# Kernel optimization log

Hardware: AMD Instinct MI355X
Metric: run time of the kernel (lower is better)

The kernel has to match this reference:

```python
import jax, jax.numpy as jnp
import numpy as np

N_NODES = 100000
N_EDGES = 1600000
N_FEAT = 128
HIDDEN = 128
N_CLASSES = 40


def gcn_conv(x, W, b, src, dst, norm, n):
    # PyG GCNConv: linear (no bias) -> gather src -> scale by sym norm -> scatter-add to dst -> + bias
    h = x @ W                      # [N, out]
    m = h[src] * norm[:, None]     # [E+N, out] gathered, normalized messages
    out = jax.ops.segment_sum(m, dst, num_segments=n)
    return out + b


def setup_inputs() -> dict:
    key = jax.random.key(0)
    ks = jax.random.split(key, 10)
    x = jax.random.normal(ks[0], (N_NODES, N_FEAT), dtype=jnp.float32)
    edge_index = jax.random.randint(ks[1], (2, N_EDGES), 0, N_NODES, dtype=jnp.int32)

    def lin(k, fan_in, fan_out):
        s = 1.0 / np.sqrt(fan_in)
        return (jax.random.uniform(k, (fan_in, fan_out), jnp.float32, -s, s))

    return {
        "x": x,
        "edge_index": edge_index,
        "W1": lin(ks[2], N_FEAT, HIDDEN), "b1": jnp.zeros((HIDDEN,), jnp.float32),
        "W2": lin(ks[3], HIDDEN, HIDDEN), "b2": jnp.zeros((HIDDEN,), jnp.float32),
        "W3": lin(ks[4], HIDDEN, HIDDEN), "b3": jnp.zeros((HIDDEN,), jnp.float32),
        "W4": lin(ks[5], HIDDEN, N_CLASSES), "b4": jnp.zeros((N_CLASSES,), jnp.float32),
    }


def reference(x, edge_index, W1, b1, W2, b2, W3, b3, W4, b4):
    n = x.shape[0]
    # add self-loops (PyG GCNConv default)
    loops = jnp.arange(n, dtype=edge_index.dtype)
    src = jnp.concatenate([edge_index[0], loops])
    dst = jnp.concatenate([edge_index[1], loops])
    # symmetric degree normalization: deg computed on destination index
    deg = jax.ops.segment_sum(jnp.ones_like(dst, x.dtype), dst, num_segments=n)
    dinv = jnp.where(deg > 0, jax.lax.rsqrt(deg), 0.0)
    norm = dinv[src] * dinv[dst]

    h = jax.nn.relu(gcn_conv(x, W1, b1, src, dst, norm, n))   # dropout = identity (eval)
    h = jax.nn.relu(gcn_conv(h, W2, b2, src, dst, norm, n))
    h = jax.nn.relu(gcn_conv(h, W3, b3, src, dst, norm, n))
    x_latent = h
    out = gcn_conv(h, W4, b4, src, dst, norm, n)
    return out, x_latent
```

## Files before the change

kernel.cpp:

```cpp
#include <hip/hip_runtime.h>
#include <hip/hip_bf16.h>
#include <hip/hip_fp16.h>


#define N_NODES 100000
#define N_EDGES 1600000

#define BSHIFT 7
#define BWIDTH 128
#define CELL_CAP 512
#define P1_EPT 16
#define P1_CHUNK 4096

typedef short s16x8 __attribute__((ext_vector_type(8)));
typedef _Float16 f16x8 __attribute__((ext_vector_type(8)));
typedef float f32x4 __attribute__((ext_vector_type(4)));
typedef float f32x2 __attribute__((ext_vector_type(2)));


__global__ __launch_bounds__(256) void pass1_bucket(const int* __restrict__ src,
                                                    const int* __restrict__ dst,
                                                    int* __restrict__ bcur2,
                                                    int2* __restrict__ cells,
                                                    int2* __restrict__ spill,
                                                    int* __restrict__ spillCnt,
                                                    int nb, int e) {
    __shared__ int hist[1024];
    __shared__ int base[1024];
    int t = threadIdx.x;
    int x = blockIdx.x & 7;
    int e0 = blockIdx.x * P1_CHUNK;

    for (int i = t; i < nb; i += 256) hist[i] = 0;
    __syncthreads();

    int ds[P1_EPT], ss[P1_EPT];
#pragma unroll
    for (int j = 0; j < P1_EPT; j++) {
        int i = e0 + j * 256 + t;
        if (i < e) {
            ds[j] = dst[i];
            ss[j] = src[i];
            atomicAdd(&hist[ds[j] >> BSHIFT], 1);
        } else {
            ds[j] = -1;
        }
    }
    __syncthreads();

    for (int i = t; i < nb; i += 256) {
        int h = hist[i];
        base[i] = (h > 0) ? atomicAdd(&bcur2[i * 8 + x], h) : 0;
        hist[i] = 0;
    }
    __syncthreads();

#pragma unroll
    for (int j = 0; j < P1_EPT; j++) {
        if (ds[j] >= 0) {
            int b = ds[j] >> BSHIFT;
            int r = atomicAdd(&hist[b], 1);
            int slot = base[b] + r;
            if (slot < CELL_CAP) {
                cells[(size_t)(b * 8 + x) * CELL_CAP + slot] = make_int2(ss[j], ds[j]);
            } else {
                int sp = atomicAdd(spillCnt, 1);
                spill[sp] = make_int2(ss[j], ds[j]);
            }
        }
    }
}

__global__ __launch_bounds__(256) void count_cells(const int* __restrict__ bcur2,
                                                   const int2* __restrict__ cells,
                                                   const int2* __restrict__ spill,
                                                   const int* __restrict__ spillCnt,
                                                   int* __restrict__ counts,
                                                   float* __restrict__ dinv,
                                                   int n) {
    __shared__ int cnt[BWIDTH];
    int b = blockIdx.x;
    int t = threadIdx.x;
    int nodeBase = b << BSHIFT;
    if (t < BWIDTH) cnt[t] = 0;
    __syncthreads();
    for (int x = 0; x < 8; x++) {
        int c = bcur2[b * 8 + x];
        if (c > CELL_CAP) c = CELL_CAP;
        const int2* cp = cells + (size_t)(b * 8 + x) * CELL_CAP;
        for (int s = t; s < c; s += 256) {
            atomicAdd(&cnt[cp[s].y - nodeBase], 1);
        }
    }
    int sc = *spillCnt;
    for (int s = t; s < sc; s += 256) {
        int d = spill[s].y;
        if ((d >> BSHIFT) == b) atomicAdd(&cnt[d - nodeBase], 1);
    }
    __syncthreads();
    if (t < BWIDTH) {
        int node = nodeBase + t;
        if (node < n) {
            int deg = cnt[t] + 1;
            counts[node] = deg;
            dinv[node] = 1.0f / sqrtf((float)deg);
        }
    }
}

__global__ __launch_bounds__(256) void scan_phase1(const int* __restrict__ counts,
                                                   int* __restrict__ blockSums, int n) {
    __shared__ int red[256];
    int t = threadIdx.x;
    int base = blockIdx.x * 1024 + t * 4;
    int s = 0;
    if (base + 3 < n) {
        int4 v = *(const int4*)(counts + base);
        s = ((v.x + 2) & ~3) + ((v.y + 2) & ~3) + ((v.z + 2) & ~3) + ((v.w + 2) & ~3);
    } else {
        for (int j = 0; j < 4; j++) if (base + j < n) s += (counts[base + j] + 2) & ~3;
    }
    red[t] = s;
    __syncthreads();
    for (int off = 128; off > 0; off >>= 1) {
        if (t < off) red[t] += red[t + off];
        __syncthreads();
    }
    if (t == 0) blockSums[blockIdx.x] = red[0];
}

__global__ __launch_bounds__(1024) void scan_phase2(int* __restrict__ blockSums, int nb) {
    __shared__ int sh[1024];
    int t = threadIdx.x;
    sh[t] = (t < nb) ? blockSums[t] : 0;
    __syncthreads();
    for (int off = 1; off < 1024; off <<= 1) {
        int v = (t >= off) ? sh[t - off] : 0;
        __syncthreads();
        sh[t] += v;
        __syncthreads();
    }
    if (t < nb) blockSums[t] = (t == 0) ? 0 : sh[t - 1];
}

__global__ __launch_bounds__(256) void scan_phase3(const int* __restrict__ counts,
                                                   const int* __restrict__ blockSums,
                                                   int* __restrict__ offsets, int n) {
    __shared__ int red[256];
    int t = threadIdx.x;
    int base = blockIdx.x * 1024 + t * 4;
    int c[4];
#pragma unroll
    for (int j = 0; j < 4; j++) c[j] = (base + j < n) ? ((counts[base + j] + 2) & ~3) : 0;
    int s = c[0] + c[1] + c[2] + c[3];
    red[t] = s;
    __syncthreads();
    for (int off = 1; off < 256; off <<= 1) {
        int v = (t >= off) ? red[t - off] : 0;
        __syncthreads();
        red[t] += v;
        __syncthreads();
    }
    int prefix = blockSums[blockIdx.x] + ((t == 0) ? 0 : red[t - 1]);
#pragma unroll
    for (int j = 0; j < 4; j++) {
        if (base + j < n) offsets[base + j] = prefix;
        prefix += c[j];
        if (base + j == n - 1) offsets[n] = prefix;
    }
}

__global__ __launch_bounds__(256) void pass2_scatter(const int* __restrict__ bcur2,
                                                     const int2* __restrict__ cells,
                                                     const int2* __restrict__ spill,
                                                     const int* __restrict__ spillCnt,
                                                     const int* __restrict__ offsets,
                                                     int* __restrict__ srcSorted, int n) {
    __shared__ int cur[BWIDTH];
    int b = blockIdx.x;
    int t = threadIdx.x;
    int nodeBase = b << BSHIFT;
    if (t < BWIDTH) cur[t] = 0;
    __syncthreads();
    for (int x = 0; x < 8; x++) {
        int c = bcur2[b * 8 + x];
        if (c > CELL_CAP) c = CELL_CAP;
        const int2* cp = cells + (size_t)(b * 8 + x) * CELL_CAP;
        for (int s = t; s < c; s += 256) {
            int2 p = cp[s];
            int r = atomicAdd(&cur[p.y - nodeBase], 1);
            srcSorted[offsets[p.y] + r] = p.x;
        }
    }
    int sc = *spillCnt;
    for (int s = t; s < sc; s += 256) {
        int2 p = spill[s];
        if ((p.y >> BSHIFT) == b) {
            int r = atomicAdd(&cur[p.y - nodeBase], 1);
            srcSorted[offsets[p.y] + r] = p.x;
        }
    }
    __syncthreads();
    if (t < BWIDTH) {
        int node = nodeBase + t;
        if (node < n) {
            int beg = offsets[node] + cur[t];
            int end = offsets[node + 1];
            for (int k = beg; k < end; k++) srcSorted[k] = n;
        }
    }
}


__device__ inline void split_bf16(float f, unsigned short& h, unsigned short& l) {
    unsigned u = __float_as_uint(f);
    unsigned hr = (u + 0x7FFFu + ((u >> 16) & 1u)) >> 16;
    h = (unsigned short)hr;
    float r = f - __uint_as_float(hr << 16);
    unsigned v = __float_as_uint(r);
    unsigned lr = (v + 0x7FFFu + ((v >> 16) & 1u)) >> 16;
    l = (unsigned short)lr;
}

__global__ __launch_bounds__(256) void prep_wfrag(const float* __restrict__ W,
                                                  short* __restrict__ wh,
                                                  short* __restrict__ wl,
                                                  __half* __restrict__ zrow) {
    if (zrow != nullptr && blockIdx.x == 0 && threadIdx.x < 64) {
        ((__half2*)zrow)[threadIdx.x] = __floats2half2_rn(0.f, 0.f);
    }
    int idx = blockIdx.x * 256 + threadIdx.x;
    int j    = idx & 7;
    int lane = (idx >> 3) & 63;
    int c    = (idx >> 9) & 3;
    int t    = idx >> 11;
    int quad = lane >> 4;
    int n = (t << 4) | (lane & 15);
    int k = (c << 5) + (quad << 3) + j;
    unsigned short h, l;
    split_bf16(W[k * 128 + n], h, l);
    wh[idx] = (short)h;
    wl[idx] = (short)l;
}

__global__ __launch_bounds__(256) void prep_wfrag16(const float* __restrict__ W,
                                                    _Float16* __restrict__ wh,
                                                    _Float16* __restrict__ wl) {
    int idx = blockIdx.x * 256 + threadIdx.x;
    int j    = idx & 7;
    int lane = (idx >> 3) & 63;
    int c    = (idx >> 9) & 3;
    int t    = idx >> 11;
    int quad = lane >> 4;
    int n = (t << 4) | (lane & 15);
    int k = (c << 5) + (quad << 3) + j;
    float v = W[k * 128 + n];
    _Float16 h = (_Float16)v;
    _Float16 l = (_Float16)((v - (float)h) * 2048.0f);
    wh[idx] = h;
    wl[idx] = l;
}


#define GEMM_GX 512

__global__ __launch_bounds__(256) void gemm_mfma(const float* __restrict__ A,
                                                 const short* __restrict__ wh,
                                                 const short* __restrict__ wl,
                                                 const float* __restrict__ dinv,
                                                 __half* __restrict__ C, int M) {
    int wv   = threadIdx.x >> 6;
    int lane = threadIdx.x & 63;
    int quad = lane >> 4;
    int mm   = lane & 15;
    int tbase = blockIdx.y * 4;

    s16x8 whf[4][4], wlf[4][4];
#pragma unroll
    for (int tt = 0; tt < 4; tt++)
#pragma unroll
        for (int c = 0; c < 4; c++) {
            int base = ((((tbase + tt) << 2) + c) << 6 | lane) << 3;
            whf[tt][c] = *(const s16x8*)(wh + base);
            wlf[tt][c] = *(const s16x8*)(wl + base);
        }

    int nStrips = M >> 4;
    for (int s = blockIdx.x * 4 + wv; s < nStrips; s += GEMM_GX * 4) {
        const float* ap = A + (size_t)((s << 4) + mm) * 128 + (quad << 3);
        f32x4 acc[4];
#pragma unroll
        for (int tt = 0; tt < 4; tt++) acc[tt] = (f32x4){0.f, 0.f, 0.f, 0.f};

#pragma unroll
        for (int c = 0; c < 4; c++) {
            float av[8];
            *(float4*)&av[0] = *(const float4*)(ap + (c << 5));
            *(float4*)&av[4] = *(const float4*)(ap + (c << 5) + 4);
            union { s16x8 v; unsigned short u[8]; } ah, al;
#pragma unroll
            for (int j = 0; j < 8; j++) split_bf16(av[j], ah.u[j], al.u[j]);
#pragma unroll
            for (int tt = 0; tt < 4; tt++) {
                acc[tt] = __builtin_amdgcn_mfma_f32_16x16x32_bf16(ah.v, whf[tt][c], acc[tt], 0, 0, 0);
                acc[tt] = __builtin_amdgcn_mfma_f32_16x16x32_bf16(ah.v, wlf[tt][c], acc[tt], 0, 0, 0);
                acc[tt] = __builtin_amdgcn_mfma_f32_16x16x32_bf16(al.v, whf[tt][c], acc[tt], 0, 0, 0);
                acc[tt] = __builtin_amdgcn_mfma_f32_16x16x32_bf16(al.v, wlf[tt][c], acc[tt], 0, 0, 0);
            }
        }
        int rbase = (s << 4) + (quad << 2);
        float dv[4];
#pragma unroll
        for (int r = 0; r < 4; r++) dv[r] = dinv[rbase + r];
        __half* cp = C + (size_t)rbase * 128 + (tbase << 4) + mm;
#pragma unroll
        for (int tt = 0; tt < 4; tt++) {
#pragma unroll
            for (int r = 0; r < 4; r++) {
                cp[(size_t)r * 128 + (tt << 4)] = __float2half(acc[tt][r] * dv[r]);
            }
        }
    }
}


__global__ __launch_bounds__(256) void gemm_mfma_f16(const __half* __restrict__ A,
                                                     const _Float16* __restrict__ wh,
                                                     const _Float16* __restrict__ wl,
                                                     const float* __restrict__ dinv,
                                                     __half* __restrict__ C, int M) {
    int wv   = threadIdx.x >> 6;
    int lane = threadIdx.x & 63;
    int quad = lane >> 4;
    int mm   = lane & 15;
    int tbase = blockIdx.y * 4;

    f16x8 whf[4][4], wlf[4][4];
#pragma unroll
    for (int tt = 0; tt < 4; tt++)
#pragma unroll
        for (int c = 0; c < 4; c++) {
            int base = ((((tbase + tt) << 2) + c) << 6 | lane) << 3;
            whf[tt][c] = *(const f16x8*)(wh + base);
            wlf[tt][c] = *(const f16x8*)(wl + base);
        }

    int nStrips = M >> 4;
    for (int s = blockIdx.x * 4 + wv; s < nStrips; s += GEMM_GX * 4) {
        const _Float16* ap = (const _Float16*)A + (size_t)((s << 4) + mm) * 128 + (quad << 3);
        f32x4 acch[4], accl[4];
#pragma unroll
        for (int tt = 0; tt < 4; tt++) {
            acch[tt] = (f32x4){0.f, 0.f, 0.f, 0.f};
            accl[tt] = (f32x4){0.f, 0.f, 0.f, 0.f};
        }

#pragma unroll
        for (int c = 0; c < 4; c++) {
            f16x8 av = *(const f16x8*)(ap + (c << 5));
#pragma unroll
            for (int tt = 0; tt < 4; tt++) {
                acch[tt] = __builtin_amdgcn_mfma_f32_16x16x32_f16(av, whf[tt][c], acch[tt], 0, 0, 0);
                accl[tt] = __builtin_amdgcn_mfma_f32_16x16x32_f16(av, wlf[tt][c], accl[tt], 0, 0, 0);
            }
        }
        int rbase = (s << 4) + (quad << 2);
        float dv[4];
#pragma unroll
        for (int r = 0; r < 4; r++) dv[r] = dinv[rbase + r];
        __half* cp = C + (size_t)rbase * 128 + (tbase << 4) + mm;
#pragma unroll
        for (int tt = 0; tt < 4; tt++) {
#pragma unroll
            for (int r = 0; r < 4; r++) {
                float v = acch[tt][r] + accl[tt][r] * (1.0f / 2048.0f);
                cp[(size_t)r * 128 + (tt << 4)] = __float2half(v * dv[r]);
            }
        }
    }
}


__global__ __launch_bounds__(320) void gemm_f32_40(const float* __restrict__ A,
                                                   const float* __restrict__ B,
                                                   const float* __restrict__ dinv,
                                                   __half* __restrict__ C, int M) {
    __shared__ float Ws[128][40];
    __shared__ float Xs[32][132];
    int t = threadIdx.x;
    int block_row = blockIdx.x * 32;

    for (int i = t; i < 128 * 40; i += 320) ((float*)Ws)[i] = B[i];
    for (int idx = t; idx < 1024; idx += 320) {
        int row = idx >> 5;
        int k4  = (idx & 31) << 2;
        int gr = block_row + row; if (gr >= M) gr = M - 1;
        float4 v = *(const float4*)(A + (size_t)gr * 128 + k4);
        *(float4*)&Xs[row][k4] = v;
    }
    __syncthreads();

    int r  = t / 10;
    int c0 = (t % 10) * 4;
    float4 acc = make_float4(0.f, 0.f, 0.f, 0.f);
    for (int k = 0; k < 128; k += 4) {
        float4 xv = *(const float4*)&Xs[r][k];
#pragma unroll
        for (int j = 0; j < 4; j++) {
            float xj = (j == 0) ? xv.x : (j == 1) ? xv.y : (j == 2) ? xv.z : xv.w;
            float4 wv = *(const float4*)&Ws[k + j][c0];
            acc.x += xj * wv.x; acc.y += xj * wv.y;
            acc.z += xj * wv.z; acc.w += xj * wv.w;
        }
    }
    int gr = block_row + r;
    if (gr < M) {
        float dv = dinv[gr];
        __half2* p = (__half2*)(C + (size_t)gr * 40 + c0);
        p[0] = __floats2half2_rn(dv * acc.x, dv * acc.y);
        p[1] = __floats2half2_rn(dv * acc.z, dv * acc.w);
    } else if (gr == M) {
        __half2* p = (__half2*)(C + (size_t)gr * 40 + c0);
        p[0] = __floats2half2_rn(0.f, 0.f);
        p[1] = __floats2half2_rn(0.f, 0.f);
    }
}


__device__ inline f32x2 h2f(__half2 v) {
    float2 t = __half22float2(v);
    return (f32x2){t.x, t.y};
}

template <int NF, bool RELU, typename OT>
__global__ __launch_bounds__(256) void agg_kernel(const __half* __restrict__ h,
                                                  const float* __restrict__ dinv,
                                                  const int* __restrict__ offsets,
                                                  const int* __restrict__ srcSorted,
                                                  const float* __restrict__ bias,
                                                  OT* __restrict__ out, int n) {
    int wave = threadIdx.x >> 6;
    int lane = threadIdx.x & 63;
    int node = blockIdx.x * 4 + wave;
    if (node >= n) return;

    int f = lane * 2;
    bool act = (f < NF);
    float di = dinv[node];
    const char* hb = (const char*)h;
    const unsigned RB = NF * 2;
    unsigned fb = (unsigned)f * 2;

    f32x2 a0 = (f32x2){0.f, 0.f}, a1 = a0, a2 = a0, a3 = a0;
    if (act) {
        a0 = h2f(*(const __half2*)(hb + (unsigned)node * RB + fb));
    }

    int idx = offsets[node];
    int end = offsets[node + 1];

    int4 sA, sB;
    bool have8 = (idx + 8 <= end);
    if (have8) {
        sA = *(const int4*)(srcSorted + idx);
        sB = *(const int4*)(srcSorted + idx + 4);
    }
    while (have8) {
        int4 cA = sA, cB = sB;
        int nidx = idx + 8;
        bool nxt = (nidx + 8 <= end);
        if (nxt) {
            sA = *(const int4*)(srcSorted + nidx);
            sB = *(const int4*)(srcSorted + nidx + 4);
        }
        if (act) {
            __half2 v0 = *(const __half2*)(hb + (unsigned)cA.x * RB + fb);
            __half2 v1 = *(const __half2*)(hb + (unsigned)cA.y * RB + fb);
            __half2 v2 = *(const __half2*)(hb + (unsigned)cA.z * RB + fb);
            __half2 v3 = *(const __half2*)(hb + (unsigned)cA.w * RB + fb);
            __half2 v4 = *(const __half2*)(hb + (unsigned)cB.x * RB + fb);
            __half2 v5 = *(const __half2*)(hb + (unsigned)cB.y * RB + fb);
            __half2 v6 = *(const __half2*)(hb + (unsigned)cB.z * RB + fb);
            __half2 v7 = *(const __half2*)(hb + (unsigned)cB.w * RB + fb);
            a0 += h2f(v0); a1 += h2f(v1); a2 += h2f(v2); a3 += h2f(v3);
            a0 += h2f(v4); a1 += h2f(v5); a2 += h2f(v6); a3 += h2f(v7);
        }
        idx = nidx;
        have8 = nxt;
    }
    if (idx + 4 <= end) {
        int4 cA = *(const int4*)(srcSorted + idx);
        if (act) {
            __half2 v0 = *(const __half2*)(hb + (unsigned)cA.x * RB + fb);
            __half2 v1 = *(const __half2*)(hb + (unsigned)cA.y * RB + fb);
            __half2 v2 = *(const __half2*)(hb + (unsigned)cA.z * RB + fb);
            __half2 v3 = *(const __half2*)(hb + (unsigned)cA.w * RB + fb);
            a0 += h2f(v0); a1 += h2f(v1); a2 += h2f(v2); a3 += h2f(v3);
        }
    }

    if (act) {
        f32x2 s = (a0 + a1) + (a2 + a3);
        float ox = di * s.x + bias[f];
        float oy = di * s.y + bias[f + 1];
        if (RELU) { ox = fmaxf(ox, 0.f); oy = fmaxf(oy, 0.f); }
        if constexpr (sizeof(OT) == 2) {
            *(__half2*)(out + (size_t)node * NF + f) = __floats2half2_rn(ox, oy);
        } else {
            *(float2*)(out + (size_t)node * NF + f) = make_float2(ox, oy);
        }
    }
}

__global__ __launch_bounds__(256) void agg40_tri(const __half* __restrict__ h,
                                                 const float* __restrict__ dinv,
                                                 const int* __restrict__ offsets,
                                                 const int* __restrict__ srcSorted,
                                                 const float* __restrict__ bias,
                                                 float* __restrict__ out, int n) {
    int wave = threadIdx.x >> 6;
    int lane = threadIdx.x & 63;
    unsigned sub = (unsigned)lane / 20u;
    int fi = lane - (int)sub * 20;
    bool act = (sub < 3u);
    int f = fi * 2;
    unsigned fb = (unsigned)fi * 4u;
    const char* hb = (const char*)h;
    float bx = act ? bias[f] : 0.f;
    float by = act ? bias[f + 1] : 0.f;
    int ntri = (n + 2) / 3;

    for (int p = blockIdx.x * 4 + wave; p < ntri; p += gridDim.x * 4) {
        int node = p * 3 + (int)sub;
        bool on = act && (node < n);
        float di = on ? dinv[node] : 0.f;
        int idx = on ? offsets[node] : 0;
        int end = on ? offsets[node + 1] : 0;

        f32x2 z = (f32x2){0.f, 0.f};
        f32x2 a0 = z, a1 = z, a2 = z, a3 = z;
        if (on) a0 = h2f(*(const __half2*)(hb + (unsigned)node * 80u + fb));

        while (__any(idx + 8 <= end)) {
            bool c = (idx + 8 <= end);
            if (c) {
                int4 sA = *(const int4*)(srcSorted + idx);
                int4 sB = *(const int4*)(srcSorted + idx + 4);
                a0 += h2f(*(const __half2*)(hb + (unsigned)sA.x * 80u + fb));
                a1 += h2f(*(const __half2*)(hb + (unsigned)sA.y * 80u + fb));
                a2 += h2f(*(const __half2*)(hb + (unsigned)sA.z * 80u + fb));
                a3 += h2f(*(const __half2*)(hb + (unsigned)sA.w * 80u + fb));
                a0 += h2f(*(const __half2*)(hb + (unsigned)sB.x * 80u + fb));
                a1 += h2f(*(const __half2*)(hb + (unsigned)sB.y * 80u + fb));
                a2 += h2f(*(const __half2*)(hb + (unsigned)sB.z * 80u + fb));
                a3 += h2f(*(const __half2*)(hb + (unsigned)sB.w * 80u + fb));
                idx += 8;
            }
        }
        if (idx + 4 <= end) {
            int4 sA = *(const int4*)(srcSorted + idx);
            a0 += h2f(*(const __half2*)(hb + (unsigned)sA.x * 80u + fb));
            a1 += h2f(*(const __half2*)(hb + (unsigned)sA.y * 80u + fb));
            a2 += h2f(*(const __half2*)(hb + (unsigned)sA.z * 80u + fb));
            a3 += h2f(*(const __half2*)(hb + (unsigned)sA.w * 80u + fb));
        }

        if (on) {
            f32x2 s = (a0 + a1) + (a2 + a3);
            float ox = di * s.x + bx;
            float oy = di * s.y + by;
            *(float2*)(out + (size_t)node * 40 + f) = make_float2(ox, oy);
        }
    }
}


extern "C" void kernel_launch(void* const* d_in, const int* in_sizes, int n_in,
                              void* d_out, int out_size, void* d_ws, size_t ws_size,
                              hipStream_t stream) {
    const float* x  = (const float*)d_in[0];
    const int* edge = (const int*)d_in[1];
    const float* W1 = (const float*)d_in[2]; const float* b1 = (const float*)d_in[3];
    const float* W2 = (const float*)d_in[4]; const float* b2 = (const float*)d_in[5];
    const float* W3 = (const float*)d_in[6]; const float* b3 = (const float*)d_in[7];
    const float* W4 = (const float*)d_in[8]; const float* b4 = (const float*)d_in[9];

    const int N = in_sizes[0] / 128;
    const int E = in_sizes[1] / 2;
    const int* src = edge;
    const int* dst = edge + E;

    float* out_final = (float*)d_out;
    float* x_latent  = (float*)d_out + (size_t)N * 40;

    const int nbk = (N + BWIDTH - 1) >> BSHIFT;

    char* w = (char*)d_ws;
    int* counts    = (int*)w;  w += (size_t)N * 4;
    int* offsets   = (int*)w;  w += (size_t)(N + 4) * 4;
    float* dinv    = (float*)w; w += (size_t)N * 4;
    int* srcSorted = (int*)w;  w += (size_t)(E + 4 * N) * 4;
    int* blockSums = (int*)w;  w += (size_t)1024 * 4;
    int* bcur2     = (int*)w;  w += (size_t)8448 * 4;
    int* spillCnt  = (int*)w;  w += (size_t)64 * 4;
    short* wfrag   = (short*)w;    w += (size_t)2 * 16384 * 2;
    _Float16* wf16 = (_Float16*)w; w += (size_t)4 * 16384 * 2;
    w = (char*)(((uintptr_t)w + 255) & ~(uintptr_t)255);
    __half* hA   = (__half*)w; w += (size_t)(N + 1) * 128 * 2;
    __half* hB16 = (__half*)w; w += (size_t)N * 128 * 2;

    int2* cells = (int2*)hA;
    int2* spill = cells + (size_t)nbk * 8 * CELL_CAP;

    short* wh1 = wfrag;            short* wl1 = wfrag + 16384;
    _Float16* wh2 = wf16;          _Float16* wl2 = wf16 + 16384;
    _Float16* wh3 = wf16 + 32768;  _Float16* wl3 = wf16 + 49152;

    int nb = (N + 1023) / 1024;
    int p1b = (E + P1_CHUNK - 1) / P1_CHUNK;

    hipMemsetAsync(bcur2, 0, (size_t)(8448 + 64) * 4, stream);
    pass1_bucket<<<p1b, 256, 0, stream>>>(src, dst, bcur2, cells, spill, spillCnt, nbk, E);
    count_cells<<<nbk, 256, 0, stream>>>(bcur2, cells, spill, spillCnt, counts, dinv, N);
    scan_phase1<<<nb, 256, 0, stream>>>(counts, blockSums, N);
    scan_phase2<<<1, 1024, 0, stream>>>(blockSums, nb);
    scan_phase3<<<nb, 256, 0, stream>>>(counts, blockSums, offsets, N);
    pass2_scatter<<<nbk, 256, 0, stream>>>(bcur2, cells, spill, spillCnt, offsets, srcSorted, N);

    prep_wfrag<<<64, 256, 0, stream>>>(W1, wh1, wl1, hA + (size_t)N * 128);
    prep_wfrag16<<<64, 256, 0, stream>>>(W2, wh2, wl2);
    prep_wfrag16<<<64, 256, 0, stream>>>(W3, wh3, wl3);

    dim3 gGemm(GEMM_GX, 2);
    int gAgg = (N + 3) / 4;

    gemm_mfma<<<gGemm, 256, 0, stream>>>(x, wh1, wl1, dinv, hA, N);
    agg_kernel<128, true, __half><<<gAgg, 256, 0, stream>>>(hA, dinv, offsets, srcSorted, b1, hB16, N);
    gemm_mfma_f16<<<gGemm, 256, 0, stream>>>(hB16, wh2, wl2, dinv, hA, N);
    agg_kernel<128, true, __half><<<gAgg, 256, 0, stream>>>(hA, dinv, offsets, srcSorted, b2, hB16, N);
    gemm_mfma_f16<<<gGemm, 256, 0, stream>>>(hB16, wh3, wl3, dinv, hA, N);
    agg_kernel<128, true, float><<<gAgg, 256, 0, stream>>>(hA, dinv, offsets, srcSorted, b3, x_latent, N);
    gemm_f32_40<<<(N + 1 + 31) / 32, 320, 0, stream>>>(x_latent, W4, dinv, hA, N);
    agg40_tri<<<2048, 256, 0, stream>>>(hA, dinv, offsets, srcSorted, b4, out_final, N);
}
```

Baseline: 486.0 us.

## Slice 128-wide aggregation into four feature slices with four nodes per wave

Replaces the one-node-per-wave aggregation with a kernel where each block covers 16 nodes and one of four 32-feature slices. Each 16-lane group in a wave handles a different node's 64-byte slice, so a wave has four independent edge lists in flight and consecutive slice blocks reuse the same rows through the cache. The goal is more memory-level parallelism and better L2 locality for the random gathers. In exchange, each edge index is reloaded four times, the per-lane prefetch of indices is gone, and lanes go idle while waiting on the node with the highest degree in their wave.

After: 605.0 us. 1.24x slower.

```diff
diff --git a/kernel.cpp b/kernel.cpp
--- a/kernel.cpp
+++ b/kernel.cpp
@@ -432,82 +432,68 @@
     return (f32x2){t.x, t.y};
 }
 
-template <int NF, bool RELU, typename OT>
-__global__ __launch_bounds__(256) void agg_kernel(const __half* __restrict__ h,
-                                                  const float* __restrict__ dinv,
-                                                  const int* __restrict__ offsets,
-                                                  const int* __restrict__ srcSorted,
-                                                  const float* __restrict__ bias,
-                                                  OT* __restrict__ out, int n) {
+template <bool RELU, typename OT>
+__global__ __launch_bounds__(256) void agg128_sliced(const __half* __restrict__ h,
+                                                     const float* __restrict__ dinv,
+                                                     const int* __restrict__ offsets,
+                                                     const int* __restrict__ srcSorted,
+                                                     const float* __restrict__ bias,
+                                                     OT* __restrict__ out, int n) {
+    int slice = blockIdx.x & 3;
+    int nodeBase = (blockIdx.x >> 2) << 4;
     int wave = threadIdx.x >> 6;
     int lane = threadIdx.x & 63;
-    int node = blockIdx.x * 4 + wave;
-    if (node >= n) return;
-
-    int f = lane * 2;
-    bool act = (f < NF);
-    float di = dinv[node];
+    int sub  = lane >> 4;
+    int fl   = lane & 15;
+    int node = nodeBase + (wave << 2) + sub;
+    bool on = (node < n);
+
     const char* hb = (const char*)h;
-    const unsigned RB = NF * 2;
-    unsigned fb = (unsigned)f * 2;
-
-    f32x2 a0 = (f32x2){0.f, 0.f}, a1 = a0, a2 = a0, a3 = a0;
-    if (act) {
-        a0 = h2f(*(const __half2*)(hb + (unsigned)node * RB + fb));
-    }
-
-    int idx = offsets[node];
-    int end = offsets[node + 1];
-
-    int4 sA, sB;
-    bool have8 = (idx + 8 <= end);
-    if (have8) {
-        sA = *(const int4*)(srcSorted + idx);
-        sB = *(const int4*)(srcSorted + idx + 4);
-    }
-    while (have8) {
-        int4 cA = sA, cB = sB;
-        int nidx = idx + 8;
-        bool nxt = (nidx + 8 <= end);
-        if (nxt) {
-            sA = *(const int4*)(srcSorted + nidx);
-            sB = *(const int4*)(srcSorted + nidx + 4);
-        }
-        if (act) {
-            __half2 v0 = *(const __half2*)(hb + (unsigned)cA.x * RB + fb);
-            __half2 v1 = *(const __half2*)(hb + (unsigned)cA.y * RB + fb);
-            __half2 v2 = *(const __half2*)(hb + (unsigned)cA.z * RB + fb);
-            __half2 v3 = *(const __half2*)(hb + (unsigned)cA.w * RB + fb);
-            __half2 v4 = *(const __half2*)(hb + (unsigned)cB.x * RB + fb);
-            __half2 v5 = *(const __half2*)(hb + (unsigned)cB.y * RB + fb);
-            __half2 v6 = *(const __half2*)(hb + (unsigned)cB.z * RB + fb);
-            __half2 v7 = *(const __half2*)(hb + (unsigned)cB.w * RB + fb);
-            a0 += h2f(v0); a1 += h2f(v1); a2 += h2f(v2); a3 += h2f(v3);
-            a0 += h2f(v4); a1 += h2f(v5); a2 += h2f(v6); a3 += h2f(v7);
-        }
-        idx = nidx;
-        have8 = nxt;
+    unsigned fb = ((unsigned)slice << 6) + ((unsigned)fl << 2);
+    int f = (slice << 5) + (fl << 1);
+    float2 bv = *(const float2*)(bias + f);
+
+    float di = on ? dinv[node] : 0.f;
+    int idx = on ? offsets[node] : 0;
+    int end = on ? offsets[node + 1] : 0;
+
+    f32x2 z = (f32x2){0.f, 0.f};
+    f32x2 a0 = z, a1 = z, a2 = z, a3 = z;
+    if (on) a0 = h2f(*(const __half2*)(hb + (unsigned)node * 256u + fb));
+
+    while (__any(idx + 8 <= end)) {
+        bool c = (idx + 8 <= end);
+        if (c) {
+            int4 sA = *(const int4*)(srcSorted + idx);
+            int4 sB = *(const int4*)(srcSorted + idx + 4);
+            a0 += h2f(*(const __half2*)(hb + (unsigned)sA.x * 256u + fb));
+            a1 += h2f(*(const __half2*)(hb + (unsigned)sA.y * 256u + fb));
+            a2 += h2f(*(const __half2*)(hb + (unsigned)sA.z * 256u + fb));
+            a3 += h2f(*(const __half2*)(hb + (unsigned)sA.w * 256u + fb));
+            a0 += h2f(*(const __half2*)(hb + (unsigned)sB.x * 256u + fb));
+            a1 += h2f(*(const __half2*)(hb + (unsigned)sB.y * 256u + fb));
+            a2 += h2f(*(const __half2*)(hb + (unsigned)sB.z * 256u + fb));
+            a3 += h2f(*(const __half2*)(hb + (unsigned)sB.w * 256u + fb));
+            idx += 8;
+        }
     }
     if (idx + 4 <= end) {
-        int4 cA = *(const int4*)(srcSorted + idx);
-        if (act) {
-            __half2 v0 = *(const __half2*)(hb + (unsigned)cA.x * RB + fb);
-            __half2 v1 = *(const __half2*)(hb + (unsigned)cA.y * RB + fb);
-            __half2 v2 = *(const __half2*)(hb + (unsigned)cA.z * RB + fb);
-            __half2 v3 = *(const __half2*)(hb + (unsigned)cA.w * RB + fb);
-            a0 += h2f(v0); a1 += h2f(v1); a2 += h2f(v2); a3 += h2f(v3);
-        }
-    }
-
-    if (act) {
+        int4 sA = *(const int4*)(srcSorted + idx);
+        a0 += h2f(*(const __half2*)(hb + (unsigned)sA.x * 256u + fb));
+        a1 += h2f(*(const __half2*)(hb + (unsigned)sA.y * 256u + fb));
+        a2 += h2f(*(const __half2*)(hb + (unsigned)sA.z * 256u + fb));
+        a3 += h2f(*(const __half2*)(hb + (unsigned)sA.w * 256u + fb));
+    }
+
+    if (on) {
         f32x2 s = (a0 + a1) + (a2 + a3);
-        float ox = di * s.x + bias[f];
-        float oy = di * s.y + bias[f + 1];
+        float ox = di * s.x + bv.x;
+        float oy = di * s.y + bv.y;
         if (RELU) { ox = fmaxf(ox, 0.f); oy = fmaxf(oy, 0.f); }
         if constexpr (sizeof(OT) == 2) {
-            *(__half2*)(out + (size_t)node * NF + f) = __floats2half2_rn(ox, oy);
+            *(__half2*)(out + (size_t)node * 128 + f) = __floats2half2_rn(ox, oy);
         } else {
-            *(float2*)(out + (size_t)node * NF + f) = make_float2(ox, oy);
+            *(float2*)(out + (size_t)node * 128 + f) = make_float2(ox, oy);
         }
     }
 }
@@ -632,14 +618,14 @@
     prep_wfrag16<<<64, 256, 0, stream>>>(W3, wh3, wl3);
 
     dim3 gGemm(GEMM_GX, 2);
-    int gAgg = (N + 3) / 4;
+    int gAggS = 4 * ((N + 15) / 16);
 
     gemm_mfma<<<gGemm, 256, 0, stream>>>(x, wh1, wl1, dinv, hA, N);
-    agg_kernel<128, true, __half><<<gAgg, 256, 0, stream>>>(hA, dinv, offsets, srcSorted, b1, hB16, N);
+    agg128_sliced<true, __half><<<gAggS, 256, 0, stream>>>(hA, dinv, offsets, srcSorted, b1, hB16, N);
     gemm_mfma_f16<<<gGemm, 256, 0, stream>>>(hB16, wh2, wl2, dinv, hA, N);
-    agg_kernel<128, true, __half><<<gAgg, 256, 0, stream>>>(hA, dinv, offsets, srcSorted, b2, hB16, N);
+    agg128_sliced<true, __half><<<gAggS, 256, 0, stream>>>(hA, dinv, offsets, srcSorted, b2, hB16, N);
     gemm_mfma_f16<<<gGemm, 256, 0, stream>>>(hB16, wh3, wl3, dinv, hA, N);
-    agg_kernel<128, true, float><<<gAgg, 256, 0, stream>>>(hA, dinv, offsets, srcSorted, b3, x_latent, N);
+    agg128_sliced<true, float><<<gAggS, 256, 0, stream>>>(hA, dinv, offsets, srcSorted, b3, x_latent, N);
     gemm_f32_40<<<(N + 1 + 31) / 32, 320, 0, stream>>>(x_latent, W4, dinv, hA, N);
     agg40_tri<<<2048, 256, 0, stream>>>(hA, dinv, offsets, srcSorted, b4, out_final, N);
 }
```
